# Kernel tuning notes

Measured on AMD Instinct MI355X. Metric: run time of the kernel, lower is better.

Reference implementation:

```python
import jax, jax.numpy as jnp
import numpy as np

N_NODES = 100000
N_EDGES = 3200000
N_GRAPHS = 1000
HID = 64
L = 4  # num_unit


def setup_inputs() -> dict:
    key = jax.random.key(0)
    ks = jax.random.split(key, 16)
    x = jax.random.normal(ks[0], (N_NODES, 4), dtype=jnp.float32)
    edge_index = jax.random.randint(ks[1], (2, N_EDGES), 0, N_NODES, dtype=jnp.int64)
    edge_attr = jax.random.uniform(ks[2], (N_EDGES,), dtype=jnp.float32)
    batch = jnp.sort(jax.random.randint(ks[3], (N_NODES,), 0, N_GRAPHS, dtype=jnp.int64))
    s = 1.0 / np.sqrt(HID)
    inp = {
        'x': x, 'edge_index': edge_index, 'edge_attr': edge_attr, 'batch': batch,
        'emb_w': jax.random.normal(ks[4], (4, HID), jnp.float32) * 0.5,
        'emb_b': jnp.zeros((HID,), jnp.float32),
        'conv_w1': jax.random.normal(ks[5], (L, HID, HID), jnp.float32) * s,
        'conv_b1': jnp.zeros((L, HID), jnp.float32),
        'conv_w2': jax.random.normal(ks[6], (L, HID, HID), jnp.float32) * s,
        'conv_w3': jax.random.normal(ks[7], (L, HID, HID), jnp.float32) * s,
        'conv_b3': jnp.zeros((L, HID), jnp.float32),
        'lin1_w': jax.random.normal(ks[8], (HID, HID), jnp.float32) * s,
        'lin1_b': jnp.zeros((HID,), jnp.float32),
        'lin2_w': jax.random.normal(ks[9], (HID, 3), jnp.float32) * s,
        'lin2_b': jnp.zeros((3,), jnp.float32),
    }
    return inp


def _forward(x, edge_index, edge_attr, batch,
             emb_w, emb_b, conv_w1, conv_b1, conv_w2, conv_w3, conv_b3,
             lin1_w, lin1_b, lin2_w, lin2_b):
    src, dst = edge_index[0], edge_index[1]
    ew = edge_attr[:, None]  # [E,1]
    h = x @ emb_w + emb_b  # node_emb; dropout omitted (eval mode)
    for l in range(conv_w1.shape[0]):
        # LEConv: out_i = sum_{j->i} w_ji * (lin1(x_j) - lin2(x_i)) + lin3(x_i)
        a = h @ conv_w1[l] + conv_b1[l]
        b = h @ conv_w2[l]  # no bias
        msg = (a[src] - b[dst]) * ew  # [E, HID]
        agg = jax.ops.segment_sum(msg, dst, num_segments=h.shape[0])
        h = jax.nn.relu(agg + h @ conv_w3[l] + conv_b3[l])
    # global mean pool over graphs
    sums = jax.ops.segment_sum(h, batch, num_segments=N_GRAPHS)
    cnt = jax.ops.segment_sum(jnp.ones((h.shape[0],), h.dtype), batch, num_segments=N_GRAPHS)
    graph_x = sums / jnp.maximum(cnt, 1.0)[:, None]
    pred = jax.nn.relu(graph_x @ lin1_w + lin1_b) @ lin2_w + lin2_b
    return pred


def reference(x, edge_index, edge_attr, batch, emb_w, emb_b,
              conv_w1, conv_b1, conv_w2, conv_w3, conv_b3,
              lin1_w, lin1_b, lin2_w, lin2_b):
    return _forward(x, edge_index, edge_attr, batch, emb_w, emb_b,
                    conv_w1, conv_b1, conv_w2, conv_w3, conv_b3,
                    lin1_w, lin1_b, lin2_w, lin2_b)
```

## Files before the change

### kernel.cpp

```cpp
#include <hip/hip_runtime.h>

#define N_NODES 100000
#define N_EDGES 3200000
#define N_GRAPHS 1000
#define NLAYER 4
#define NB 391
#define G1 782
#define EPB 4096
#define PCAP 16384

typedef __attribute__((ext_vector_type(8))) short bf16x8;
typedef __attribute__((ext_vector_type(4))) float f32x4;

static __device__ __forceinline__ unsigned f2bf(float f) {
  unsigned u = __float_as_uint(f);
  return (u + 0x7fffu + ((u >> 16) & 1u)) >> 16;
}
static __device__ __forceinline__ float bf2f_lo(unsigned u) {
  return __uint_as_float(u << 16);
}
static __device__ __forceinline__ float bf2f_hi(unsigned u) {
  return __uint_as_float(u & 0xffff0000u);
}

__global__ __launch_bounds__(256) void embed_kernel(
    const float* __restrict__ x, const float* __restrict__ emb_w,
    const float* __restrict__ emb_b, unsigned short* __restrict__ h_bf)
{
  int t = blockIdx.x * 256 + threadIdx.x;
  if (t >= N_NODES * 64) return;
  int c = t & 63, v = t >> 6;
  float4 xv = ((const float4*)x)[v];
  float acc = emb_b[c];
  acc = fmaf(xv.x, emb_w[0 * 64 + c], acc);
  acc = fmaf(xv.y, emb_w[1 * 64 + c], acc);
  acc = fmaf(xv.z, emb_w[2 * 64 + c], acc);
  acc = fmaf(xv.w, emb_w[3 * 64 + c], acc);
  h_bf[t] = (unsigned short)f2bf(acc);
}

__global__ __launch_bounds__(256) void bhist_kernel(
    const int* __restrict__ ei, int* __restrict__ bhist)
{
  __shared__ unsigned hist[NB];
  for (int i = threadIdx.x; i < NB; i += 256) hist[i] = 0;
  __syncthreads();
  int base = blockIdx.x * EPB;
#pragma unroll
  for (int i = 0; i < 16; ++i) {
    int e = base + i * 256 + threadIdx.x;
    if (e < N_EDGES) atomicAdd(&hist[((unsigned)ei[N_EDGES + e]) >> 8], 1u);
  }
  __syncthreads();
  for (int i = threadIdx.x; i < NB; i += 256)
    bhist[blockIdx.x * NB + i] = (int)hist[i];
}

__global__ __launch_bounds__(256) void colscan_kernel(
    int* __restrict__ bhist, int* __restrict__ tots)
{
  int b = blockIdx.x;
  __shared__ int s[256];
  __shared__ int carry;
  if (threadIdx.x == 0) carry = 0;
  __syncthreads();
  for (int c0 = 0; c0 < G1; c0 += 256) {
    int g = c0 + threadIdx.x;
    int v = (g < G1) ? bhist[g * NB + b] : 0;
    s[threadIdx.x] = v;
    __syncthreads();
    for (int off = 1; off < 256; off <<= 1) {
      int y = (threadIdx.x >= off) ? s[threadIdx.x - off] : 0;
      __syncthreads();
      s[threadIdx.x] += y;
      __syncthreads();
    }
    if (g < G1) bhist[g * NB + b] = carry + s[threadIdx.x] - v;
    __syncthreads();
    if (threadIdx.x == 0) carry += s[255];
    __syncthreads();
  }
  if (threadIdx.x == 0) tots[b] = carry;
}

__global__ __launch_bounds__(512) void bucketscan_kernel(
    const int* __restrict__ tots, int* __restrict__ bb)
{
  __shared__ int s[512];
  int x = ((int)threadIdx.x < NB) ? tots[threadIdx.x] : 0;
  s[threadIdx.x] = x;
  __syncthreads();
  for (int off = 1; off < 512; off <<= 1) {
    int y = (threadIdx.x >= off) ? s[threadIdx.x - off] : 0;
    __syncthreads();
    s[threadIdx.x] += y;
    __syncthreads();
  }
  if ((int)threadIdx.x < NB) bb[threadIdx.x] = s[threadIdx.x] - x;
  if (threadIdx.x == 0) bb[NB] = N_EDGES;
}

__global__ __launch_bounds__(256) void bscatter_kernel(
    const int* __restrict__ ei, const float* __restrict__ ea,
    const int* __restrict__ bhist, const int* __restrict__ bb,
    int2* __restrict__ tmp)
{
  __shared__ unsigned hist[NB];
  __shared__ int lbase[NB];
  __shared__ unsigned cur[NB];
  __shared__ int2 stage[EPB];
  __shared__ unsigned short bid[EPB];
  __shared__ int carry;
  __shared__ int sbuf[256];
  int tid = threadIdx.x;
  int base = blockIdx.x * EPB;

  for (int i = tid; i < NB; i += 256) hist[i] = 0;
  if (tid == 0) carry = 0;
  __syncthreads();

#pragma unroll
  for (int i = 0; i < 16; ++i) {
    int e = base + i * 256 + tid;
    if (e < N_EDGES) atomicAdd(&hist[((unsigned)ei[N_EDGES + e]) >> 8], 1u);
  }
  __syncthreads();

  for (int c0 = 0; c0 < NB; c0 += 256) {
    int g = c0 + tid;
    int v = (g < NB) ? (int)hist[g] : 0;
    sbuf[tid] = v;
    __syncthreads();
    for (int off = 1; off < 256; off <<= 1) {
      int y = (tid >= off) ? sbuf[tid - off] : 0;
      __syncthreads();
      sbuf[tid] += y;
      __syncthreads();
    }
    if (g < NB) {
      int ex = carry + sbuf[tid] - v;
      lbase[g] = ex;
      cur[g] = (unsigned)ex;
    }
    __syncthreads();
    if (tid == 0) carry += sbuf[255];
    __syncthreads();
  }

#pragma unroll
  for (int i = 0; i < 16; ++i) {
    int e = base + i * 256 + tid;
    if (e < N_EDGES) {
      int d = ei[N_EDGES + e];
      unsigned bkt = ((unsigned)d) >> 8;
      unsigned lp = atomicAdd(&cur[bkt], 1u);
      stage[lp] = make_int2(ei[e] | ((d & 255) << 17), __float_as_int(ea[e]));
      bid[lp] = (unsigned short)bkt;
    }
  }
  __syncthreads();

  int nE = min(EPB, N_EDGES - base);
  for (int i = tid; i < nE; i += 256) {
    int bkt = (int)bid[i];
    int gpos = bb[bkt] + bhist[blockIdx.x * NB + bkt] + (i - lbase[bkt]);
    tmp[gpos] = stage[i];
  }
}

__global__ __launch_bounds__(256) void bucket_sort_kernel(
    const int* __restrict__ bb, const int2* __restrict__ tmp,
    unsigned* __restrict__ csr, int* __restrict__ row_off, float* __restrict__ degw)
{
  int j = blockIdx.x;
  int b0 = bb[j], b1 = bb[j + 1];
  int nE = b1 - b0;
  __shared__ unsigned hist[256];
  __shared__ float dws[256];
  __shared__ int scanbuf[256];
  __shared__ unsigned cur[256];
  __shared__ unsigned short perm[PCAP];
  int t = threadIdx.x;
  hist[t] = 0;
  dws[t] = 0.f;
  __syncthreads();
  for (int i = t; i < nE; i += 256) {
    int2 r = tmp[b0 + i];
    int bin = ((unsigned)r.x) >> 17;
    atomicAdd(&hist[bin], 1u);
    atomicAdd(&dws[bin], __int_as_float(r.y));
  }
  __syncthreads();
  int v = (int)hist[t];
  scanbuf[t] = v;
  __syncthreads();
  for (int off = 1; off < 256; off <<= 1) {
    int y = (t >= off) ? scanbuf[t - off] : 0;
    __syncthreads();
    scanbuf[t] += y;
    __syncthreads();
  }
  int myexcl = scanbuf[t] - v;
  cur[t] = (unsigned)myexcl;
  int vnode = (j << 8) + t;
  if (vnode < N_NODES) {
    row_off[vnode] = b0 + myexcl;
    degw[vnode] = dws[t];
  }
  if (j == NB - 1 && t == 0) row_off[N_NODES] = N_EDGES;
  __syncthreads();

  if (nE <= PCAP) {
    for (int i = t; i < nE; i += 256) {
      int2 r = tmp[b0 + i];
      int bin = ((unsigned)r.x) >> 17;
      unsigned p = atomicAdd(&cur[bin], 1u);
      perm[p] = (unsigned short)i;
    }
    __syncthreads();
    for (int q = t; q < nE; q += 256) {
      int2 r = tmp[b0 + (int)perm[q]];
      unsigned q15 = (unsigned)(__int_as_float(r.y) * 32768.0f);
      csr[b0 + q] = ((unsigned)r.x & 0x1FFFFu) | (q15 << 17);
    }
  } else {
    for (int i = t; i < nE; i += 256) {
      int2 r = tmp[b0 + i];
      int bin = ((unsigned)r.x) >> 17;
      unsigned p = atomicAdd(&cur[bin], 1u);
      unsigned q15 = (unsigned)(__int_as_float(r.y) * 32768.0f);
      csr[b0 + (int)p] = ((unsigned)r.x & 0x1FFFFu) | (q15 << 17);
    }
  }
}

__global__ __launch_bounds__(256) void matvec3_mfma_kernel(
    const unsigned short* __restrict__ h_bf,
    const float* __restrict__ w1, const float* __restrict__ b1,
    const float* __restrict__ w2,
    const float* __restrict__ w3, const float* __restrict__ b3,
    const float* __restrict__ degw,
    unsigned short* __restrict__ a_bf, unsigned short* __restrict__ cc_bf)
{
  __shared__ unsigned wfrag[6144];
  int tid = threadIdx.x;
  {
    int n = tid & 63;
    int gofs = tid >> 6;
    for (int it = 0; it < 24; ++it) {
      int g = it * 4 + gofs;
      int m = g >> 5;
      int kp = g & 31;
      int k = kp * 2;
      const float* W = (m == 0) ? w2 : (m == 1) ? w3 : w1;
      unsigned lo = f2bf(W[k * 64 + n]);
      unsigned hi = f2bf(W[(k + 1) * 64 + n]);
      int c = k >> 5;
      int kk = k & 31;
      int lane = ((kk >> 3) << 4) | (n & 15);
      int j2 = (kk & 7) >> 1;
      int t = n >> 4;
      wfrag[(((m * 2 + c) * 4 + t) << 8) | (lane << 2) | j2] = lo | (hi << 16);
    }
  }
  __syncthreads();

  int wave = tid >> 6;
  int lane = tid & 63;
  int quad = lane >> 4;
  int col = lane & 15;

#pragma unroll
  for (int tt = 0; tt < 4; ++tt) {
    int nb = blockIdx.x * 256 + wave * 64 + tt * 16;
    int arow = nb + col;
    if (arow >= N_NODES) arow = N_NODES - 1;
    const bf16x8* ap = (const bf16x8*)(h_bf + (size_t)arow * 64 + quad * 8);
    bf16x8 af0 = ap[0];
    bf16x8 af1 = ap[4];

    float dwr[4];
#pragma unroll
    for (int r = 0; r < 4; ++r) {
      int row = nb + quad * 4 + r;
      dwr[r] = degw[row < N_NODES ? row : 0];
    }

#pragma unroll
    for (int t = 0; t < 4; ++t) {
      const bf16x8* b20 = (const bf16x8*)&wfrag[((0 * 4 + t) << 8) + lane * 4];
      const bf16x8* b21 = (const bf16x8*)&wfrag[((1 * 4 + t) << 8) + lane * 4];
      const bf16x8* b30 = (const bf16x8*)&wfrag[((2 * 4 + t) << 8) + lane * 4];
      const bf16x8* b31 = (const bf16x8*)&wfrag[((3 * 4 + t) << 8) + lane * 4];
      const bf16x8* b10 = (const bf16x8*)&wfrag[((4 * 4 + t) << 8) + lane * 4];
      const bf16x8* b11 = (const bf16x8*)&wfrag[((5 * 4 + t) << 8) + lane * 4];

      f32x4 z = {0.f, 0.f, 0.f, 0.f};
      f32x4 acc2 = __builtin_amdgcn_mfma_f32_16x16x32_bf16(af0, *b20, z, 0, 0, 0);
      acc2 = __builtin_amdgcn_mfma_f32_16x16x32_bf16(af1, *b21, acc2, 0, 0, 0);
      f32x4 cc;
#pragma unroll
      for (int r = 0; r < 4; ++r) cc[r] = -dwr[r] * acc2[r];
      cc = __builtin_amdgcn_mfma_f32_16x16x32_bf16(af0, *b30, cc, 0, 0, 0);
      cc = __builtin_amdgcn_mfma_f32_16x16x32_bf16(af1, *b31, cc, 0, 0, 0);
      float bb3 = b3[t * 16 + col];
#pragma unroll
      for (int r = 0; r < 4; ++r) {
        int row = nb + quad * 4 + r;
        if (row < N_NODES)
          cc_bf[(size_t)row * 64 + t * 16 + col] = (unsigned short)f2bf(cc[r] + bb3);
      }

      float bb1 = b1[t * 16 + col];
      f32x4 a1 = {bb1, bb1, bb1, bb1};
      a1 = __builtin_amdgcn_mfma_f32_16x16x32_bf16(af0, *b10, a1, 0, 0, 0);
      a1 = __builtin_amdgcn_mfma_f32_16x16x32_bf16(af1, *b11, a1, 0, 0, 0);
#pragma unroll
      for (int r = 0; r < 4; ++r) {
        int row = nb + quad * 4 + r;
        if (row < N_NODES)
          a_bf[(size_t)row * 64 + t * 16 + col] = (unsigned short)f2bf(a1[r]);
      }
    }
  }
}

__global__ __launch_bounds__(256) void agg_kernel(
    const uint2* __restrict__ a2, const uint2* __restrict__ cc2,
    const int* __restrict__ row_off, const unsigned* __restrict__ csr,
    float4* __restrict__ h4, unsigned short* __restrict__ h_bf, int write_h)
{
  int wave = (blockIdx.x * 256 + threadIdx.x) >> 6;
  int lane = threadIdx.x & 63;
  int sg = lane >> 4;
  int li = lane & 15;
  int v = wave * 4 + sg;
  bool valid = v < N_NODES;
  int vc = valid ? v : N_NODES - 1;
  int base = row_off[vc];
  int ecnt = valid ? (row_off[vc + 1] - base) : 0;
  int emax = ecnt;
  emax = max(emax, __shfl_xor(emax, 16));
  emax = max(emax, __shfl_xor(emax, 32));

  float4 acc = make_float4(0.f, 0.f, 0.f, 0.f);
  if (valid) {
    uint2 cu = cc2[(size_t)vc * 16 + li];
    acc.x = bf2f_lo(cu.x);
    acc.y = bf2f_hi(cu.x);
    acc.z = bf2f_lo(cu.y);
    acc.w = bf2f_hi(cu.y);
  }

  int full = emax & ~15;
  int c0 = 0;
  for (; c0 < full; c0 += 16) {
    int idx = c0 + li;
    unsigned er = (idx < ecnt) ? csr[base + idx] : 0u;
#pragma unroll
    for (int j = 0; j < 16; ++j) {
      unsigned r = (unsigned)__shfl((int)er, sg * 16 + j);
      int s = (int)(r & 0x1FFFFu);
      float w = (float)(r >> 17) * (1.0f / 32768.0f);
      uint2 u = a2[(size_t)s * 16 + li];
      acc.x = fmaf(w, bf2f_lo(u.x), acc.x);
      acc.y = fmaf(w, bf2f_hi(u.x), acc.y);
      acc.z = fmaf(w, bf2f_lo(u.y), acc.z);
      acc.w = fmaf(w, bf2f_hi(u.y), acc.w);
    }
  }
  int rem = emax - full;
  if (rem > 0) {
    int idx = c0 + li;
    unsigned er = (idx < ecnt) ? csr[base + idx] : 0u;
    for (int j = 0; j < rem; ++j) {
      unsigned r = (unsigned)__shfl((int)er, sg * 16 + j);
      int s = (int)(r & 0x1FFFFu);
      float w = (float)(r >> 17) * (1.0f / 32768.0f);
      uint2 u = a2[(size_t)s * 16 + li];
      acc.x = fmaf(w, bf2f_lo(u.x), acc.x);
      acc.y = fmaf(w, bf2f_hi(u.x), acc.y);
      acc.z = fmaf(w, bf2f_lo(u.y), acc.z);
      acc.w = fmaf(w, bf2f_hi(u.y), acc.w);
    }
  }
  if (valid) {
    acc.x = fmaxf(acc.x, 0.f);
    acc.y = fmaxf(acc.y, 0.f);
    acc.z = fmaxf(acc.z, 0.f);
    acc.w = fmaxf(acc.w, 0.f);
    if (write_h) h4[(size_t)v * 16 + li] = acc;
    uint2 p;
    p.x = f2bf(acc.x) | (f2bf(acc.y) << 16);
    p.y = f2bf(acc.z) | (f2bf(acc.w) << 16);
    ((uint2*)h_bf)[(size_t)v * 16 + li] = p;
  }
}

__global__ __launch_bounds__(256) void head_kernel(
    const float* __restrict__ h, const int* __restrict__ batch,
    const float* __restrict__ l1w, const float* __restrict__ l1b,
    const float* __restrict__ l2w, const float* __restrict__ l2b,
    float* __restrict__ out)
{
  int g = (blockIdx.x * 256 + threadIdx.x) >> 6;
  int lane = threadIdx.x & 63;
  if (g >= N_GRAPHS) return;
  int lo = 0, hi = N_NODES;
  while (lo < hi) { int mid = (lo + hi) >> 1; if (batch[mid] < g) lo = mid + 1; else hi = mid; }
  int start = lo;
  hi = N_NODES;
  while (lo < hi) { int mid = (lo + hi) >> 1; if (batch[mid] < g + 1) lo = mid + 1; else hi = mid; }
  int end = lo;

  float sum = 0.f;
  for (int v = start; v < end; ++v) sum += h[(size_t)v * 64 + lane];
  float cntf = (float)(end - start);
  float gx = sum / fmaxf(cntf, 1.f);

  float acc = l1b[lane];
  for (int k = 0; k < 64; ++k) {
    float gxk = __shfl(gx, k);
    acc = fmaf(gxk, l1w[k * 64 + lane], acc);
  }
  float t = fmaxf(acc, 0.f);
  float p0 = t * l2w[lane * 3 + 0];
  float p1 = t * l2w[lane * 3 + 1];
  float p2 = t * l2w[lane * 3 + 2];
  for (int off = 32; off > 0; off >>= 1) {
    p0 += __shfl_down(p0, off);
    p1 += __shfl_down(p1, off);
    p2 += __shfl_down(p2, off);
  }
  if (lane == 0) {
    out[g * 3 + 0] = p0 + l2b[0];
    out[g * 3 + 1] = p1 + l2b[1];
    out[g * 3 + 2] = p2 + l2b[2];
  }
}

extern "C" void kernel_launch(void* const* d_in, const int* in_sizes, int n_in,
                              void* d_out, int out_size, void* d_ws, size_t ws_size,
                              hipStream_t stream)
{
  (void)in_sizes; (void)n_in; (void)out_size; (void)ws_size;
  const float* x     = (const float*)d_in[0];
  const int*   ei    = (const int*)d_in[1];
  const float* ea    = (const float*)d_in[2];
  const int*   batch = (const int*)d_in[3];
  const float* emb_w = (const float*)d_in[4];
  const float* emb_b = (const float*)d_in[5];
  const float* cw1   = (const float*)d_in[6];
  const float* cb1   = (const float*)d_in[7];
  const float* cw2   = (const float*)d_in[8];
  const float* cw3   = (const float*)d_in[9];
  const float* cb3   = (const float*)d_in[10];
  const float* l1w   = (const float*)d_in[11];
  const float* l1b   = (const float*)d_in[12];
  const float* l2w   = (const float*)d_in[13];
  const float* l2b   = (const float*)d_in[14];
  float* out = (float*)d_out;

  char* wsb = (char*)d_ws;
  size_t off = 0;
  auto alloc = [&](size_t bytes) {
    char* p = wsb + off;
    off = (off + bytes + 255) & ~(size_t)255;
    return p;
  };
  float* h       = (float*)alloc(sizeof(float) * (size_t)N_NODES * 64);
  unsigned short* h_bf = (unsigned short*)alloc(sizeof(short) * (size_t)N_NODES * 64);
  unsigned short* a_bf = (unsigned short*)alloc(sizeof(short) * (size_t)N_NODES * 64);
  unsigned short* cc_bf = (unsigned short*)alloc(sizeof(short) * (size_t)N_NODES * 64);
  unsigned* csr  = (unsigned*)alloc(sizeof(unsigned) * (size_t)N_EDGES);
  int*   row_off = (int*)alloc(sizeof(int) * (N_NODES + 1));
  float* degw    = (float*)alloc(sizeof(float) * N_NODES);
  int*   bhist   = (int*)alloc(sizeof(int) * (size_t)G1 * NB);
  int*   tots    = (int*)alloc(sizeof(int) * NB);
  int*   bb      = (int*)alloc(sizeof(int) * (NB + 1));
  int2* tmp = (int2*)h;

  embed_kernel<<<(N_NODES * 64 + 255) / 256, 256, 0, stream>>>(x, emb_w, emb_b, h_bf);
  bhist_kernel<<<G1, 256, 0, stream>>>(ei, bhist);
  colscan_kernel<<<NB, 256, 0, stream>>>(bhist, tots);
  bucketscan_kernel<<<1, 512, 0, stream>>>(tots, bb);
  bscatter_kernel<<<G1, 256, 0, stream>>>(ei, ea, bhist, bb, tmp);
  bucket_sort_kernel<<<NB, 256, 0, stream>>>(bb, tmp, csr, row_off, degw);

  int agg_blocks = (N_NODES + 15) / 16;
  int mv_blocks = (N_NODES + 255) / 256;
  for (int l = 0; l < NLAYER; ++l) {
    matvec3_mfma_kernel<<<mv_blocks, 256, 0, stream>>>(
        h_bf, cw1 + l * 4096, cb1 + l * 64, cw2 + l * 4096, cw3 + l * 4096,
        cb3 + l * 64, degw, a_bf, cc_bf);
    agg_kernel<<<agg_blocks, 256, 0, stream>>>(
        (const uint2*)a_bf, (const uint2*)cc_bf, row_off, csr, (float4*)h,
        h_bf, (l == NLAYER - 1) ? 1 : 0);
  }

  head_kernel<<<(N_GRAPHS * 64 + 255) / 256, 256, 0, stream>>>(
      h, batch, l1w, l1b, l2w, l2b, out);
}
```

Baseline: 537.9 us.

## Process 8 nodes per wave in aggregation with 16-byte gathers; halve matvec tile

The aggregation kernel now assigns 8 lanes per destination node, each handling 8 features through 16-byte uint4 gathers, instead of 16 lanes with 8-byte loads. Each wave therefore covers 8 nodes, so fewer, wider gather instructions are issued per edge. The CSR chunk of 16 edges is split into two 8-lane halves. The matvec kernel separately processes 128 nodes per block instead of 256, doubling its block count. The aggregation change adds register pressure and makes more divergence across the 8 nodes sharing a wave likely.

```diff
diff --git a/kernel.cpp b/kernel.cpp
--- a/kernel.cpp
+++ b/kernel.cpp
@@ -271,8 +271,8 @@
   int col = lane & 15;
 
 #pragma unroll
-  for (int tt = 0; tt < 4; ++tt) {
-    int nb = blockIdx.x * 256 + wave * 64 + tt * 16;
+  for (int tt = 0; tt < 2; ++tt) {
+    int nb = blockIdx.x * 128 + wave * 32 + tt * 16;
     int arow = nb + col;
     if (arow >= N_NODES) arow = N_NODES - 1;
     const bf16x8* ap = (const bf16x8*)(h_bf + (size_t)arow * 64 + quad * 8);
@@ -326,74 +326,87 @@
 }
 
 __global__ __launch_bounds__(256) void agg_kernel(
-    const uint2* __restrict__ a2, const uint2* __restrict__ cc2,
+    const uint4* __restrict__ a4, const uint4* __restrict__ cc4,
     const int* __restrict__ row_off, const unsigned* __restrict__ csr,
-    float4* __restrict__ h4, unsigned short* __restrict__ h_bf, int write_h)
+    float4* __restrict__ h4, uint4* __restrict__ hbf4, int write_h)
 {
   int wave = (blockIdx.x * 256 + threadIdx.x) >> 6;
   int lane = threadIdx.x & 63;
-  int sg = lane >> 4;
-  int li = lane & 15;
-  int v = wave * 4 + sg;
+  int sg = lane >> 3;
+  int li = lane & 7;
+  int v = wave * 8 + sg;
   bool valid = v < N_NODES;
   int vc = valid ? v : N_NODES - 1;
   int base = row_off[vc];
   int ecnt = valid ? (row_off[vc + 1] - base) : 0;
   int emax = ecnt;
+  emax = max(emax, __shfl_xor(emax, 8));
   emax = max(emax, __shfl_xor(emax, 16));
   emax = max(emax, __shfl_xor(emax, 32));
 
-  float4 acc = make_float4(0.f, 0.f, 0.f, 0.f);
+  float acc[8];
   if (valid) {
-    uint2 cu = cc2[(size_t)vc * 16 + li];
-    acc.x = bf2f_lo(cu.x);
-    acc.y = bf2f_hi(cu.x);
-    acc.z = bf2f_lo(cu.y);
-    acc.w = bf2f_hi(cu.y);
-  }
+    uint4 cu = cc4[(size_t)vc * 8 + li];
+    acc[0] = bf2f_lo(cu.x); acc[1] = bf2f_hi(cu.x);
+    acc[2] = bf2f_lo(cu.y); acc[3] = bf2f_hi(cu.y);
+    acc[4] = bf2f_lo(cu.z); acc[5] = bf2f_hi(cu.z);
+    acc[6] = bf2f_lo(cu.w); acc[7] = bf2f_hi(cu.w);
+  } else {
+#pragma unroll
+    for (int i = 0; i < 8; ++i) acc[i] = 0.f;
+  }
+
+  auto edge_mac = [&](unsigned r) {
+    int s = (int)(r & 0x1FFFFu);
+    float w = (float)(r >> 17) * (1.0f / 32768.0f);
+    uint4 u = a4[(size_t)s * 8 + li];
+    acc[0] = fmaf(w, bf2f_lo(u.x), acc[0]);
+    acc[1] = fmaf(w, bf2f_hi(u.x), acc[1]);
+    acc[2] = fmaf(w, bf2f_lo(u.y), acc[2]);
+    acc[3] = fmaf(w, bf2f_hi(u.y), acc[3]);
+    acc[4] = fmaf(w, bf2f_lo(u.z), acc[4]);
+    acc[5] = fmaf(w, bf2f_hi(u.z), acc[5]);
+    acc[6] = fmaf(w, bf2f_lo(u.w), acc[6]);
+    acc[7] = fmaf(w, bf2f_hi(u.w), acc[7]);
+  };
 
   int full = emax & ~15;
   int c0 = 0;
   for (; c0 < full; c0 += 16) {
-    int idx = c0 + li;
-    unsigned er = (idx < ecnt) ? csr[base + idx] : 0u;
-#pragma unroll
-    for (int j = 0; j < 16; ++j) {
-      unsigned r = (unsigned)__shfl((int)er, sg * 16 + j);
-      int s = (int)(r & 0x1FFFFu);
-      float w = (float)(r >> 17) * (1.0f / 32768.0f);
-      uint2 u = a2[(size_t)s * 16 + li];
-      acc.x = fmaf(w, bf2f_lo(u.x), acc.x);
-      acc.y = fmaf(w, bf2f_hi(u.x), acc.y);
-      acc.z = fmaf(w, bf2f_lo(u.y), acc.z);
-      acc.w = fmaf(w, bf2f_hi(u.y), acc.w);
-    }
+    int ia = c0 + li, ib = c0 + 8 + li;
+    unsigned erA = (ia < ecnt) ? csr[base + ia] : 0u;
+    unsigned erB = (ib < ecnt) ? csr[base + ib] : 0u;
+#pragma unroll
+    for (int j = 0; j < 8; ++j) edge_mac((unsigned)__shfl((int)erA, sg * 8 + j));
+#pragma unroll
+    for (int j = 0; j < 8; ++j) edge_mac((unsigned)__shfl((int)erB, sg * 8 + j));
   }
   int rem = emax - full;
   if (rem > 0) {
-    int idx = c0 + li;
-    unsigned er = (idx < ecnt) ? csr[base + idx] : 0u;
-    for (int j = 0; j < rem; ++j) {
-      unsigned r = (unsigned)__shfl((int)er, sg * 16 + j);
-      int s = (int)(r & 0x1FFFFu);
-      float w = (float)(r >> 17) * (1.0f / 32768.0f);
-      uint2 u = a2[(size_t)s * 16 + li];
-      acc.x = fmaf(w, bf2f_lo(u.x), acc.x);
-      acc.y = fmaf(w, bf2f_hi(u.x), acc.y);
-      acc.z = fmaf(w, bf2f_lo(u.y), acc.z);
-      acc.w = fmaf(w, bf2f_hi(u.y), acc.w);
-    }
-  }
+    int ia = c0 + li, ib = c0 + 8 + li;
+    unsigned erA = (ia < ecnt) ? csr[base + ia] : 0u;
+    unsigned erB = (ib < ecnt) ? csr[base + ib] : 0u;
+    int ra = min(rem, 8);
+    for (int j = 0; j < ra; ++j) edge_mac((unsigned)__shfl((int)erA, sg * 8 + j));
+    int rb = rem - 8;
+    for (int j = 0; j < rb; ++j) edge_mac((unsigned)__shfl((int)erB, sg * 8 + j));
+  }
+
   if (valid) {
-    acc.x = fmaxf(acc.x, 0.f);
-    acc.y = fmaxf(acc.y, 0.f);
-    acc.z = fmaxf(acc.z, 0.f);
-    acc.w = fmaxf(acc.w, 0.f);
-    if (write_h) h4[(size_t)v * 16 + li] = acc;
-    uint2 p;
-    p.x = f2bf(acc.x) | (f2bf(acc.y) << 16);
-    p.y = f2bf(acc.z) | (f2bf(acc.w) << 16);
-    ((uint2*)h_bf)[(size_t)v * 16 + li] = p;
+#pragma unroll
+    for (int i = 0; i < 8; ++i) acc[i] = fmaxf(acc[i], 0.f);
+    if (write_h) {
+      float4 lo4 = make_float4(acc[0], acc[1], acc[2], acc[3]);
+      float4 hi4 = make_float4(acc[4], acc[5], acc[6], acc[7]);
+      h4[(size_t)v * 16 + li * 2] = lo4;
+      h4[(size_t)v * 16 + li * 2 + 1] = hi4;
+    }
+    uint4 p;
+    p.x = f2bf(acc[0]) | (f2bf(acc[1]) << 16);
+    p.y = f2bf(acc[2]) | (f2bf(acc[3]) << 16);
+    p.z = f2bf(acc[4]) | (f2bf(acc[5]) << 16);
+    p.w = f2bf(acc[6]) | (f2bf(acc[7]) << 16);
+    hbf4[(size_t)v * 8 + li] = p;
   }
 }
 
@@ -487,15 +500,15 @@
   bscatter_kernel<<<G1, 256, 0, stream>>>(ei, ea, bhist, bb, tmp);
   bucket_sort_kernel<<<NB, 256, 0, stream>>>(bb, tmp, csr, row_off, degw);
 
-  int agg_blocks = (N_NODES + 15) / 16;
-  int mv_blocks = (N_NODES + 255) / 256;
+  int agg_blocks = (N_NODES + 31) / 32;
+  int mv_blocks = (N_NODES + 127) / 128;
   for (int l = 0; l < NLAYER; ++l) {
     matvec3_mfma_kernel<<<mv_blocks, 256, 0, stream>>>(
         h_bf, cw1 + l * 4096, cb1 + l * 64, cw2 + l * 4096, cw3 + l * 4096,
         cb3 + l * 64, degw, a_bf, cc_bf);
     agg_kernel<<<agg_blocks, 256, 0, stream>>>(
-        (const uint2*)a_bf, (const uint2*)cc_bf, row_off, csr, (float4*)h,
-        h_bf, (l == NLAYER - 1) ? 1 : 0);
+        (const uint4*)a_bf, (const uint4*)cc_bf, row_off, csr, (float4*)h,
+        (uint4*)h_bf, (l == NLAYER - 1) ? 1 : 0);
   }
 
   head_kernel<<<(N_GRAPHS * 64 + 255) / 256, 256, 0, stream>>>(
```

New measurement: 564.2 us. 1.05x slower.
